# Optimization experiments

Measured on AMD Instinct MI355X. Metric: run time of the kernel, lower is better.

Reference implementation:

```python
import jax, jax.numpy as jnp
import numpy as np
from jax import lax

HIDDEN_DIM = 256


def _conv(x, w, b, stride):
    # x: [B,T,H,W,Cin], w: [1,kh,kw,Cin,Cout]
    y = lax.conv_general_dilated(
        x, w, window_strides=(1, stride, stride), padding='SAME',
        dimension_numbers=('NDHWC', 'DHWIO', 'NDHWC'))
    return y + b


def _encode(video, w1, b1, w2, b2, w3, b3):
    x = video / 255.0
    x = jax.nn.relu(_conv(x, w1, b1, 2))
    x = jax.nn.relu(_conv(x, w2, b2, 2))
    x = jax.nn.relu(_conv(x, w3, b3, 2))
    return x  # [B,T,H/8,W/8,HIDDEN_DIM]


def _sample_features(features, t_idx, y_idx, x_idx):
    # Bilinear sample features[b, t_idx, y_idx, x_idx] -> [B,N,C]
    B, T, H, W, C = features.shape
    t = jnp.clip(t_idx, 0, T - 1)
    y0 = jnp.clip(jnp.floor(y_idx).astype(jnp.int32), 0, H - 1)
    y1 = jnp.clip(y0 + 1, 0, H - 1)
    x0 = jnp.clip(jnp.floor(x_idx).astype(jnp.int32), 0, W - 1)
    x1 = jnp.clip(x0 + 1, 0, W - 1)
    wy1 = y_idx - y0.astype(features.dtype)
    wy0 = 1.0 - wy1
    wx1 = x_idx - x0.astype(features.dtype)
    wx0 = 1.0 - wx1
    bi = jnp.arange(B)[:, None]
    f00 = features[bi, t, y0, x0]
    f01 = features[bi, t, y0, x1]
    f10 = features[bi, t, y1, x0]
    f11 = features[bi, t, y1, x1]
    f0 = f00 * wx0[..., None] + f01 * wx1[..., None]
    f1 = f10 * wx0[..., None] + f11 * wx1[..., None]
    return f0 * wy0[..., None] + f1 * wy1[..., None]


def _forward(video, query_points, w1, b1, w2, b2, w3, b3):
    B, T, H, W, _ = video.shape
    N = query_points.shape[1]
    x = _encode(video, w1, b1, w2, b2, w3, b3)
    feat_H, feat_W = x.shape[2], x.shape[3]
    query_t = (query_points[:, :, 0] * (T - 1)).astype(jnp.int32)
    query_y = query_points[:, :, 1] * (feat_H - 1)
    query_x = query_points[:, :, 2] * (feat_W - 1)
    q = _sample_features(x, query_t, query_y, query_x)  # [B,N,C]
    # dense correlation volume [B,N,T,fH,fW]
    corr = jnp.einsum('bnc,bthwc->bnthw', q, x) / jnp.sqrt(jnp.float32(HIDDEN_DIM))
    probs = jax.nn.softmax(corr.reshape(B, N, T, feat_H * feat_W) * 10.0, axis=-1)
    yy, xx = jnp.meshgrid(jnp.arange(feat_H, dtype=x.dtype),
                          jnp.arange(feat_W, dtype=x.dtype), indexing='ij')
    coords_flat = jnp.stack([xx.flatten(), yy.flatten()], axis=-1)  # [fH*fW, 2]
    pred = jnp.einsum('bntk,kc->bntc', probs, coords_flat)
    pred = pred.at[..., 0].set(pred[..., 0] * (W / feat_W))
    pred = pred.at[..., 1].set(pred[..., 1] * (H / feat_H))
    occlusion = jax.nn.sigmoid(-jnp.max(corr, axis=(-2, -1)))  # [B,N,T]
    return pred, occlusion


def setup_inputs() -> dict:
    key = jax.random.key(0)
    ks = jax.random.split(key, 10)
    B, T, H, W, N = 2, 24, 256, 256, 512
    video = jax.random.uniform(ks[0], (B, T, H, W, 3), jnp.float32) * 255.0
    query_points = jax.random.uniform(ks[1], (B, N, 3), jnp.float32)
    s = 0.05
    w1 = jax.random.normal(ks[2], (1, 7, 7, 3, 64), jnp.float32) * s
    b1 = jnp.zeros((64,), jnp.float32)
    w2 = jax.random.normal(ks[3], (1, 3, 3, 64, 128), jnp.float32) * s
    b2 = jnp.zeros((128,), jnp.float32)
    w3 = jax.random.normal(ks[4], (1, 3, 3, 128, HIDDEN_DIM), jnp.float32) * s
    b3 = jnp.zeros((HIDDEN_DIM,), jnp.float32)
    return {'video': video, 'query_points': query_points,
            'w1': w1, 'b1': b1, 'w2': w2, 'b2': b2, 'w3': w3, 'b3': b3}


def reference(video, query_points, w1, b1, w2, b2, w3, b3):
    return _forward(video, query_points, w1, b1, w2, b2, w3, b3)
```

## Files before the change

### kernel.cpp

```cpp
#include <hip/hip_runtime.h>
#include <hip/hip_bf16.h>
#include <cstdint>
#include <cstddef>


typedef __attribute__((ext_vector_type(8))) short bf16x8;
typedef __attribute__((ext_vector_type(4))) float f32x4;

typedef const __attribute__((address_space(1))) void gv_t;
typedef __attribute__((address_space(3))) void sv_t;

__device__ __forceinline__ unsigned short bfr(float f) {
    return (unsigned short)(__bfloat16_as_ushort(__float2bfloat16(f)));
}

__global__ __launch_bounds__(256) void k_prep(const float* __restrict__ video,
                                              const float* __restrict__ w1,
                                              const float* __restrict__ w2,
                                              const float* __restrict__ w3,
                                              __hip_bfloat16* __restrict__ pv,
                                              unsigned short* __restrict__ c1p,
                                              unsigned short* __restrict__ c2p,
                                              __hip_bfloat16* __restrict__ wp1,
                                              __hip_bfloat16* __restrict__ wp2,
                                              __hip_bfloat16* __restrict__ wp3)
{
    const int bid = blockIdx.x;
    if (bid < 12288) {
        const int iy = bid & 255;
        const int bt = bid >> 8;
        const int ix = threadIdx.x;
        const float* src = video + ((size_t)(bt * 256 + iy) * 256 + ix) * 3;
        unsigned* dst = (unsigned*)(pv + ((size_t)(bt * 261) + iy + 2) * 1056);
        const float v0 = src[0], v1 = src[1], v2 = src[2];
        const unsigned lo = (unsigned)bfr(v0) | ((unsigned)bfr(v1) << 16);
        const unsigned hi = (unsigned)bfr(v2);
        dst[(2 + ix) * 2 + 0] = lo;
        dst[(2 + ix) * 2 + 1] = hi;
        if (ix < 2)   { dst[ix * 2] = 0u; dst[ix * 2 + 1] = 0u; }
        if (ix >= 250){ dst[(ix + 8) * 2] = 0u; dst[(ix + 8) * 2 + 1] = 0u; }
    } else if (bid < 12288 + 7170) {
        const int i = (bid - 12288) * 256 + threadIdx.x;
        unsigned short* pvs = (unsigned short*)pv;
        if (i < 253440) {
            const int bt = i / 5280, rr = (i % 5280) / 1056, col = i % 1056;
            const int row = (rr < 2) ? rr : rr + 256;
            pvs[(size_t)(bt * 261 + row) * 1056 + col] = 0;
        } else if (i < 1042944) {
            const int j = i - 253440, bt = j / 16448, k = j % 16448;
            size_t addr;
            if (k < 8256) { const int px = k >> 6, c = k & 63;
                addr = ((size_t)(bt * 129 + 128) * 129 + px) * 64 + c; }
            else { const int k2 = k - 8256, row = k2 >> 6, c = k2 & 63;
                addr = ((size_t)(bt * 129 + row) * 129 + 128) * 64 + c; }
            c1p[addr] = 0;
        } else if (i < 1835520) {
            const int j = i - 1042944, bt = j / 16512, k = j % 16512;
            size_t addr;
            if (k < 8320) { const int px = k >> 7, c = k & 127;
                addr = ((size_t)(bt * 65 + 64) * 65 + px) * 128 + c; }
            else { const int k2 = k - 8320, row = k2 >> 7, c = k2 & 127;
                addr = ((size_t)(bt * 65 + row) * 65 + 64) * 128 + c; }
            c2p[addr] = 0;
        }
    } else {
        const int e = (bid - 12288 - 7170) * 256 + threadIdx.x;
        if (e < 14336) {
            const int j = e & 7, lane = (e >> 3) & 63, nt = (e >> 9) & 3, kh = e >> 11;
            const int k = ((lane >> 4) << 3) + j;
            const int kw = k >> 2, ci = k & 3;
            const int n = nt * 16 + (lane & 15);
            float v = (ci < 3 && kw < 7) ? w1[(size_t)((kh * 7 + kw) * 3 + ci) * 64 + n] : 0.f;
            wp1[e] = __float2bfloat16(v);
        } else if (e < 88064) {
            const int e2 = e - 14336;
            const int j = e2 & 7, lane = (e2 >> 3) & 63, nt = (e2 >> 9) & 7, ks = (e2 >> 12) & 1, tap = e2 >> 13;
            const int ci = ks * 32 + ((lane >> 4) << 3) + j;
            const int n  = nt * 16 + (lane & 15);
            wp2[e2] = __float2bfloat16(w2[(size_t)(tap * 64 + ci) * 128 + n]);
        } else {
            const int e3 = e - 88064;
            const int j = e3 & 7, lane = (e3 >> 3) & 63, nt = (e3 >> 9) & 15, ks = (e3 >> 13) & 3, tap = e3 >> 15;
            const int ci = ks * 32 + ((lane >> 4) << 3) + j;
            const int n  = nt * 16 + (lane & 15);
            wp3[e3] = __float2bfloat16(w3[(size_t)(tap * 128 + ci) * 256 + n]);
        }
    }
}

__global__ __launch_bounds__(256) void k_conv1m(const __hip_bfloat16* __restrict__ pv,
                                                const __hip_bfloat16* __restrict__ wp,
                                                const float* __restrict__ b1,
                                                __hip_bfloat16* __restrict__ out)
{
    const int xcd = blockIdx.x & 7;
    const int sub = blockIdx.x >> 3;
    const int bt  = xcd * 6 + (sub >> 7);
    const int oy  = sub & 127;
    const int w  = threadIdx.x >> 6;
    const int l  = threadIdx.x & 63;
    const int li = l & 15, lh = l >> 4;

    f32x4 acc[2][4];
#pragma unroll
    for (int m = 0; m < 2; ++m)
#pragma unroll
        for (int n = 0; n < 4; ++n) acc[m][n] = (f32x4){0.f, 0.f, 0.f, 0.f};

    const short* pvS = (const short*)pv;
    const short* wS  = (const short*)wp;

#pragma unroll
    for (int kh = 0; kh < 7; ++kh) {
        const short* row = pvS + (size_t)(bt * 261 + oy * 2 + kh) * 1056;
        bf16x8 bw[4];
#pragma unroll
        for (int nt = 0; nt < 4; ++nt)
            bw[nt] = *reinterpret_cast<const bf16x8*>(wS + ((size_t)(kh * 4 + nt) * 64 + l) * 8);
#pragma unroll
        for (int mt = 0; mt < 2; ++mt) {
            const int ox = w * 32 + mt * 16 + li;
            bf16x8 a = *reinterpret_cast<const bf16x8*>(row + 8 * (ox + lh));
#pragma unroll
            for (int nt = 0; nt < 4; ++nt)
                acc[mt][nt] = __builtin_amdgcn_mfma_f32_16x16x32_bf16(a, bw[nt], acc[mt][nt], 0, 0, 0);
        }
    }

    __hip_bfloat16* op = out + ((size_t)(bt * 129 + oy) * 129) * 64;
#pragma unroll
    for (int mt = 0; mt < 2; ++mt) {
        const int px0 = w * 32 + mt * 16 + lh * 4;
#pragma unroll
        for (int nt = 0; nt < 4; ++nt) {
            const int n = nt * 16 + li;
            const float bias = b1[n];
#pragma unroll
            for (int r = 0; r < 4; ++r) {
                const float v = fmaxf(acc[mt][nt][r] * (1.f / 255.f) + bias, 0.f);
                op[(size_t)(px0 + r) * 64 + n] = __float2bfloat16(v);
            }
        }
    }
}

template<int CIN, int COUT, int OW, int IW, int ORS, int NTHR, int WMT, int WNT, int MINW>
__global__ __launch_bounds__(NTHR, MINW) void k_convr(const __hip_bfloat16* __restrict__ in,
                                                      const __hip_bfloat16* __restrict__ wp,
                                                      const float* __restrict__ bias,
                                                      __hip_bfloat16* __restrict__ out)
{
    constexpr int KSN  = CIN / 32;
    constexpr int NSL  = 9 * KSN;
    constexpr int NTT  = COUT / 16;
    constexpr int GPX  = CIN / 8;
    constexpr int ROWG = IW * GPX;
    constexpr int RST  = ROWG * 16;
    constexpr int TOT  = 3 * ROWG;
    constexpr int SIT  = (TOT + NTHR - 1) / NTHR;

    __shared__ char lbuf[3 * RST];

    const int bid = blockIdx.x;
    const int xcd = bid & 7;
    const int sub = bid >> 3;
    const int bt  = xcd * 6 + sub / OW;
    const int oy  = sub % OW;

    const int tid = threadIdx.x;
    const int w   = tid >> 6;
    const int l   = tid & 63;
    const int li  = l & 15, lh = l >> 4;
    const int ntb = w * WNT;

    const short* inS = (const short*)in;
    const size_t rb = (size_t)(bt * IW + oy * 2) * IW * CIN;
#pragma unroll
    for (int it = 0; it < SIT; ++it) {
        const int g = it * NTHR + tid;
        if (g < TOT) {
            const int r  = g / ROWG;
            const int rm = g - r * ROWG;
            const int px = rm / GPX;
            const int j  = rm - px * GPX;
            const int q  = j ^ ((px >> 1) & 7);
            __builtin_amdgcn_global_load_lds(
                (gv_t*)(inS + rb + (size_t)r * IW * CIN + px * CIN + q * 8),
                (sv_t*)(lbuf + (size_t)g * 16), 16, 0, 0);
        }
    }
    __syncthreads();

    f32x4 acc[WMT][WNT];
#pragma unroll
    for (int i = 0; i < WMT; ++i)
#pragma unroll
        for (int j = 0; j < WNT; ++j) acc[i][j] = (f32x4){0.f, 0.f, 0.f, 0.f};

    const char* wB = (const char*)wp;

#pragma unroll
    for (int s = 0; s < NSL; ++s) {
        const int tap = s / KSN, ks = s % KSN;
        const int kh = tap / 3, kw = tap % 3;

        bf16x8 bf[WNT];
#pragma unroll
        for (int j = 0; j < WNT; ++j)
            bf[j] = *reinterpret_cast<const bf16x8*>(wB + ((size_t)s * NTT + ntb + j) * 1024 + l * 16);

        const char* Ar = lbuf + kh * RST;
        bf16x8 af[WMT];
#pragma unroll
        for (int i = 0; i < WMT; ++i) {
            const int ix  = (i * 16 + li) * 2 + kw;
            const int off = ((ks * 4 + lh) ^ ((ix >> 1) & 7)) * 16;
            af[i] = *reinterpret_cast<const bf16x8*>(Ar + (size_t)ix * (CIN * 2) + off);
        }

#pragma unroll
        for (int i = 0; i < WMT; ++i)
#pragma unroll
            for (int j = 0; j < WNT; ++j)
                acc[i][j] = __builtin_amdgcn_mfma_f32_16x16x32_bf16(af[i], bf[j], acc[i][j], 0, 0, 0);
    }

    __hip_bfloat16* ob = out + (size_t)(bt * ORS + oy) * ORS * COUT;
#pragma unroll
    for (int i = 0; i < WMT; ++i) {
        const int ox = i * 16 + lh * 4;
#pragma unroll
        for (int j = 0; j < WNT; ++j) {
            const int n = (ntb + j) * 16 + li;
            const float bv = bias[n];
#pragma unroll
            for (int r = 0; r < 4; ++r) {
                const float v = fmaxf(acc[i][j][r] + bv, 0.f);
                ob[(size_t)(ox + r) * COUT + n] = __float2bfloat16(v);
            }
        }
    }
}

__global__ __launch_bounds__(256) void k_sample(const float* __restrict__ qp,
                                                const __hip_bfloat16* __restrict__ feat,
                                                __hip_bfloat16* __restrict__ q)
{
    const int bn = blockIdx.x;
    const int b  = bn >> 9;
    const float t3 = qp[bn * 3 + 0];
    const float yv = qp[bn * 3 + 1] * 31.f;
    const float xv = qp[bn * 3 + 2] * 31.f;
    int t = (int)(t3 * 23.f);
    t = min(max(t, 0), 23);
    int y0 = (int)floorf(yv); y0 = min(max(y0, 0), 31);
    const int y1 = min(y0 + 1, 31);
    int x0 = (int)floorf(xv); x0 = min(max(x0, 0), 31);
    const int x1 = min(x0 + 1, 31);
    const float wy1 = yv - (float)y0, wy0 = 1.f - wy1;
    const float wx1 = xv - (float)x0, wx0 = 1.f - wx1;

    const int c = threadIdx.x;
    const __hip_bfloat16* fb = feat + ((size_t)(b * 24 + t) * 1024) * 256;
    const float f00 = __bfloat162float(fb[(size_t)(y0 * 32 + x0) * 256 + c]);
    const float f01 = __bfloat162float(fb[(size_t)(y0 * 32 + x1) * 256 + c]);
    const float f10 = __bfloat162float(fb[(size_t)(y1 * 32 + x0) * 256 + c]);
    const float f11 = __bfloat162float(fb[(size_t)(y1 * 32 + x1) * 256 + c]);
    const float v = (f00 * wx0 + f01 * wx1) * wy0 + (f10 * wx0 + f11 * wx1) * wy1;
    q[(size_t)bn * 256 + c] = __float2bfloat16(v);
}

__global__ __launch_bounds__(256, 2) void k_corrm(const __hip_bfloat16* __restrict__ qb,
                                                  const __hip_bfloat16* __restrict__ featb,
                                                  float* __restrict__ pbuf)
{
    __shared__ short lbuf[2][8192];

    const int bid = blockIdx.x;
    const int xcd = bid & 7;
    const int sub = bid >> 3;
    const int grp = sub >> 5;
    const int prt = sub & 31;
    const int img = xcd * 6 + grp;
    const int bq  = img / 24, t = img % 24;
    const int nc  = prt & 3, ps = prt >> 2;

    const int tid = threadIdx.x;
    const int w   = tid >> 6;
    const int l   = tid & 63;
    const int li  = l & 15, lh = l >> 4;

    const short* qS = (const short*)qb;
    const short* fS = (const short*)featb + (size_t)img * 1024 * 256;
    const char*  tile0 = (const char*)(fS + (size_t)(ps * 128) * 256);

    const int q0 = nc * 128 + w * 32;
    bf16x8 aq[2][8];
#pragma unroll
    for (int mt = 0; mt < 2; ++mt)
#pragma unroll
        for (int ks = 0; ks < 8; ++ks)
            aq[mt][ks] = *reinterpret_cast<const bf16x8*>(
                qS + ((size_t)(bq * 512 + q0 + mt * 16 + li)) * 256 + ks * 32 + lh * 8);

    float m[2][4], s[2][4], sx[2][4], sy[2][4], dmx[2][4];
#pragma unroll
    for (int mt = 0; mt < 2; ++mt)
#pragma unroll
        for (int r = 0; r < 4; ++r) {
            m[mt][r] = -1e30f; s[mt][r] = 0.f; sx[mt][r] = 0.f; sy[mt][r] = 0.f; dmx[mt][r] = -1e30f;
        }

    bf16x8 stg[4];
#pragma unroll
    for (int i = 0; i < 4; ++i) {
        const int g = i * 256 + tid;
        const int pos = g >> 5, kb = (g & 31) * 16;
        stg[i] = *reinterpret_cast<const bf16x8*>(tile0 + (size_t)pos * 512 + kb);
    }
#pragma unroll
    for (int i = 0; i < 4; ++i) {
        const int g = i * 256 + tid;
        const int pos = g >> 5, kb = (g & 31) * 16;
        *reinterpret_cast<bf16x8*>((char*)&lbuf[0][0] + pos * 512 + (kb ^ ((pos & 7) << 4))) = stg[i];
    }
    __syncthreads();

#pragma unroll
    for (int st = 0; st < 4; ++st) {
        const int cur = st & 1;

        if (st < 3) {
            const char* tn = tile0 + (size_t)((st + 1) * 32) * 512;
#pragma unroll
            for (int i = 0; i < 4; ++i) {
                const int g = i * 256 + tid;
                const int pos = g >> 5, kb = (g & 31) * 16;
                stg[i] = *reinterpret_cast<const bf16x8*>(tn + (size_t)pos * 512 + kb);
            }
        }

        f32x4 acc[2][2];
#pragma unroll
        for (int mt = 0; mt < 2; ++mt)
#pragma unroll
            for (int pt = 0; pt < 2; ++pt) acc[mt][pt] = (f32x4){0.f, 0.f, 0.f, 0.f};

#pragma unroll
        for (int pt = 0; pt < 2; ++pt) {
            const int p = pt * 16 + li;
#pragma unroll
            for (int ks = 0; ks < 8; ++ks) {
                const int k = ks * 32 + lh * 8;
                bf16x8 bv = *reinterpret_cast<const bf16x8*>(&lbuf[cur][p * 256 + (k ^ ((p & 7) << 3))]);
                acc[0][pt] = __builtin_amdgcn_mfma_f32_16x16x32_bf16(aq[0][ks], bv, acc[0][pt], 0, 0, 0);
                acc[1][pt] = __builtin_amdgcn_mfma_f32_16x16x32_bf16(aq[1][ks], bv, acc[1][pt], 0, 0, 0);
            }
        }

        const float py = (float)(ps * 4 + st);
#pragma unroll
        for (int mt = 0; mt < 2; ++mt)
#pragma unroll
            for (int r = 0; r < 4; ++r) {
                const float v0 = acc[mt][0][r], v1 = acc[mt][1][r];
                float mx = fmaxf(v0, v1);
                mx = fmaxf(mx, __shfl_xor(mx, 1));
                mx = fmaxf(mx, __shfl_xor(mx, 2));
                mx = fmaxf(mx, __shfl_xor(mx, 4));
                mx = fmaxf(mx, __shfl_xor(mx, 8));
                dmx[mt][r] = fmaxf(dmx[mt][r], mx);
                const float mn = fmaxf(m[mt][r], mx * 0.625f);
                const float sc = __expf(m[mt][r] - mn);
                const float e0 = __expf(v0 * 0.625f - mn);
                const float e1 = __expf(v1 * 0.625f - mn);
                const float es = e0 + e1;
                s[mt][r]  = s[mt][r]  * sc + es;
                sx[mt][r] = sx[mt][r] * sc + es * (float)li + 16.f * e1;
                sy[mt][r] = sy[mt][r] * sc + es * py;
                m[mt][r] = mn;
            }

        if (st < 3) {
#pragma unroll
            for (int i = 0; i < 4; ++i) {
                const int g = i * 256 + tid;
                const int pos = g >> 5, kb = (g & 31) * 16;
                *reinterpret_cast<bf16x8*>((char*)&lbuf[cur ^ 1][0] + pos * 512 + (kb ^ ((pos & 7) << 4))) = stg[i];
            }
            __syncthreads();
        }
    }

#pragma unroll
    for (int mt = 0; mt < 2; ++mt)
#pragma unroll
        for (int r = 0; r < 4; ++r) {
#pragma unroll
            for (int off = 1; off < 16; off <<= 1) {
                s[mt][r]  += __shfl_xor(s[mt][r],  off);
                sx[mt][r] += __shfl_xor(sx[mt][r], off);
                sy[mt][r] += __shfl_xor(sy[mt][r], off);
            }
        }

    if (li == 0) {
#pragma unroll
        for (int mt = 0; mt < 2; ++mt)
#pragma unroll
            for (int r = 0; r < 4; ++r) {
                const int n = q0 + mt * 16 + lh * 4 + r;
                const int bnt = (bq * 512 + n) * 24 + t;
                const int pi = ps * 24576 + bnt;
                pbuf[pi]                = m[mt][r];
                pbuf[196608 + pi]       = s[mt][r];
                pbuf[393216 + pi]       = sx[mt][r];
                pbuf[589824 + pi]       = sy[mt][r];
                pbuf[786432 + pi]       = dmx[mt][r];
            }
    }
}

__global__ __launch_bounds__(256) void k_merge(const float* __restrict__ pbuf,
                                               float* __restrict__ outp)
{
    const int i = blockIdx.x * 256 + threadIdx.x;
    float M = -1e30f, D = -1e30f;
#pragma unroll
    for (int ps = 0; ps < 8; ++ps) {
        M = fmaxf(M, pbuf[ps * 24576 + i]);
        D = fmaxf(D, pbuf[786432 + ps * 24576 + i]);
    }
    float s = 0.f, sx = 0.f, sy = 0.f;
#pragma unroll
    for (int ps = 0; ps < 8; ++ps) {
        const int pi = ps * 24576 + i;
        const float wgt = __expf(pbuf[pi] - M);
        s  += pbuf[196608 + pi] * wgt;
        sx += pbuf[393216 + pi] * wgt;
        sy += pbuf[589824 + pi] * wgt;
    }
    const float inv = 8.f / s;
    outp[i * 2 + 0] = sx * inv;
    outp[i * 2 + 1] = sy * inv;
    outp[49152 + i] = 1.f / (1.f + __expf(D * 0.0625f));
}

extern "C" void kernel_launch(void* const* d_in, const int* in_sizes, int n_in,
                              void* d_out, int out_size, void* d_ws, size_t ws_size,
                              hipStream_t stream)
{
    const float* video = (const float*)d_in[0];
    const float* qp    = (const float*)d_in[1];
    const float* w1    = (const float*)d_in[2];
    const float* b1    = (const float*)d_in[3];
    const float* w2    = (const float*)d_in[4];
    const float* b2    = (const float*)d_in[5];
    const float* w3    = (const float*)d_in[6];
    const float* b3    = (const float*)d_in[7];
    float* out = (float*)d_out;

    char* wsb = (char*)d_ws;
    __hip_bfloat16* c1p   = (__hip_bfloat16*)(wsb);
    __hip_bfloat16* c2p   = (__hip_bfloat16*)(wsb + 102242304ull);
    __hip_bfloat16* pv    = (__hip_bfloat16*)(wsb + 154159104ull);
    __hip_bfloat16* featb = (__hip_bfloat16*)(wsb + 154159104ull);
    __hip_bfloat16* qbuf  = (__hip_bfloat16*)(wsb + 180618240ull);
    __hip_bfloat16* w1p   = (__hip_bfloat16*)(wsb + 181142528ull);
    __hip_bfloat16* w2p   = (__hip_bfloat16*)(wsb + 181171200ull);
    __hip_bfloat16* w3p   = (__hip_bfloat16*)(wsb + 181318656ull);
    float*          pbuf  = (float*)(wsb + 181908480ull);

    k_prep      <<<dim3(20954),    dim3(256), 0, stream>>>(
                       video, w1, w2, w3, pv,
                       (unsigned short*)c1p, (unsigned short*)c2p, w1p, w2p, w3p);
    k_conv1m    <<<dim3(48 * 128), dim3(256), 0, stream>>>(pv, w1p, b1, c1p);
    k_convr<64, 128, 64, 129, 65, 256, 4, 2, 3><<<dim3(3072), dim3(256), 0, stream>>>(c1p, w2p, b2, c2p);
    k_convr<128, 256, 32, 65, 32, 512, 2, 2, 6><<<dim3(1536), dim3(512), 0, stream>>>(c2p, w3p, b3, featb);
    k_sample    <<<dim3(1024),     dim3(256), 0, stream>>>(qp, featb, qbuf);
    k_corrm     <<<dim3(1536),     dim3(256), 0, stream>>>(qbuf, featb, pbuf);
    k_merge     <<<dim3(96),       dim3(256), 0, stream>>>(pbuf, out);
}
```

Before: 189.7 us.

## Fuse conv1 and conv2 into one kernel staging conv1 rows in LDS

Conv1 and conv2 now run in one kernel. Each block computes the three conv1 output rows one conv2 output row needs and keeps them in swizzled shared memory, then runs the conv2 MFMA loop from LDS. This drops the round trip of the roughly 100 MB conv1 intermediate through global memory, plus its padding init and one launch. In exchange, conv1 rows that neighbouring output rows share (stride 2 with a 3-row window) are recomputed, roughly 1.5x the conv1 work, and about 48 KB of LDS per block limits occupancy.

```diff
diff --git a/kernel.cpp b/kernel.cpp
--- a/kernel.cpp
+++ b/kernel.cpp
@@ -19,7 +19,6 @@
                                               const float* __restrict__ w2,
                                               const float* __restrict__ w3,
                                               __hip_bfloat16* __restrict__ pv,
-                                              unsigned short* __restrict__ c1p,
                                               unsigned short* __restrict__ c2p,
                                               __hip_bfloat16* __restrict__ wp1,
                                               __hip_bfloat16* __restrict__ wp2,
@@ -39,23 +38,15 @@
         dst[(2 + ix) * 2 + 1] = hi;
         if (ix < 2)   { dst[ix * 2] = 0u; dst[ix * 2 + 1] = 0u; }
         if (ix >= 250){ dst[(ix + 8) * 2] = 0u; dst[(ix + 8) * 2 + 1] = 0u; }
-    } else if (bid < 12288 + 7170) {
+    } else if (bid < 12288 + 4086) {
         const int i = (bid - 12288) * 256 + threadIdx.x;
         unsigned short* pvs = (unsigned short*)pv;
         if (i < 253440) {
             const int bt = i / 5280, rr = (i % 5280) / 1056, col = i % 1056;
             const int row = (rr < 2) ? rr : rr + 256;
             pvs[(size_t)(bt * 261 + row) * 1056 + col] = 0;
-        } else if (i < 1042944) {
-            const int j = i - 253440, bt = j / 16448, k = j % 16448;
-            size_t addr;
-            if (k < 8256) { const int px = k >> 6, c = k & 63;
-                addr = ((size_t)(bt * 129 + 128) * 129 + px) * 64 + c; }
-            else { const int k2 = k - 8256, row = k2 >> 6, c = k2 & 63;
-                addr = ((size_t)(bt * 129 + row) * 129 + 128) * 64 + c; }
-            c1p[addr] = 0;
-        } else if (i < 1835520) {
-            const int j = i - 1042944, bt = j / 16512, k = j % 16512;
+        } else {
+            const int j = i - 253440, bt = j / 16512, k = j % 16512;
             size_t addr;
             if (k < 8320) { const int px = k >> 7, c = k & 127;
                 addr = ((size_t)(bt * 65 + 64) * 65 + px) * 128 + c; }
@@ -64,7 +55,7 @@
             c2p[addr] = 0;
         }
     } else {
-        const int e = (bid - 12288 - 7170) * 256 + threadIdx.x;
+        const int e = (bid - 12288 - 4086) * 256 + threadIdx.x;
         if (e < 14336) {
             const int j = e & 7, lane = (e >> 3) & 63, nt = (e >> 9) & 3, kh = e >> 11;
             const int k = ((lane >> 4) << 3) + j;
@@ -88,57 +79,130 @@
     }
 }
 
-__global__ __launch_bounds__(256) void k_conv1m(const __hip_bfloat16* __restrict__ pv,
-                                                const __hip_bfloat16* __restrict__ wp,
-                                                const float* __restrict__ b1,
-                                                __hip_bfloat16* __restrict__ out)
-{
+__global__ __launch_bounds__(256, 3) void k_conv12(const __hip_bfloat16* __restrict__ pv,
+                                                   const __hip_bfloat16* __restrict__ w1p,
+                                                   const float* __restrict__ b1,
+                                                   const __hip_bfloat16* __restrict__ w2p,
+                                                   const float* __restrict__ b2,
+                                                   __hip_bfloat16* __restrict__ c2p)
+{
+    __shared__ __align__(16) char lc1[3 * 16512];
+
     const int xcd = blockIdx.x & 7;
     const int sub = blockIdx.x >> 3;
-    const int bt  = xcd * 6 + (sub >> 7);
-    const int oy  = sub & 127;
-    const int w  = threadIdx.x >> 6;
-    const int l  = threadIdx.x & 63;
-    const int li = l & 15, lh = l >> 4;
-
-    f32x4 acc[2][4];
-#pragma unroll
-    for (int m = 0; m < 2; ++m)
-#pragma unroll
-        for (int n = 0; n < 4; ++n) acc[m][n] = (f32x4){0.f, 0.f, 0.f, 0.f};
+    const int bt  = xcd * 6 + sub / 64;
+    const int oy2 = sub % 64;
+    const int tid = threadIdx.x;
+    const int w   = tid >> 6;
+    const int l   = tid & 63;
+    const int li  = l & 15, lh = l >> 4;
 
     const short* pvS = (const short*)pv;
-    const short* wS  = (const short*)wp;
-
-#pragma unroll
-    for (int kh = 0; kh < 7; ++kh) {
-        const short* row = pvS + (size_t)(bt * 261 + oy * 2 + kh) * 1056;
-        bf16x8 bw[4];
-#pragma unroll
-        for (int nt = 0; nt < 4; ++nt)
-            bw[nt] = *reinterpret_cast<const bf16x8*>(wS + ((size_t)(kh * 4 + nt) * 64 + l) * 8);
-#pragma unroll
-        for (int mt = 0; mt < 2; ++mt) {
-            const int ox = w * 32 + mt * 16 + li;
-            bf16x8 a = *reinterpret_cast<const bf16x8*>(row + 8 * (ox + lh));
-#pragma unroll
-            for (int nt = 0; nt < 4; ++nt)
-                acc[mt][nt] = __builtin_amdgcn_mfma_f32_16x16x32_bf16(a, bw[nt], acc[mt][nt], 0, 0, 0);
-        }
-    }
-
-    __hip_bfloat16* op = out + ((size_t)(bt * 129 + oy) * 129) * 64;
-#pragma unroll
-    for (int mt = 0; mt < 2; ++mt) {
-        const int px0 = w * 32 + mt * 16 + lh * 4;
-#pragma unroll
-        for (int nt = 0; nt < 4; ++nt) {
-            const int n = nt * 16 + li;
-            const float bias = b1[n];
-#pragma unroll
-            for (int r = 0; r < 4; ++r) {
-                const float v = fmaxf(acc[mt][nt][r] * (1.f / 255.f) + bias, 0.f);
-                op[(size_t)(px0 + r) * 64 + n] = __float2bfloat16(v);
+    const short* w1S = (const short*)w1p;
+
+#pragma unroll
+    for (int kh2 = 0; kh2 < 3; ++kh2) {
+        const int r = oy2 * 2 + kh2;
+        char* rowbuf = lc1 + kh2 * 16512;
+        if (r < 128) {
+            f32x4 acc[2][4];
+#pragma unroll
+            for (int m = 0; m < 2; ++m)
+#pragma unroll
+                for (int n = 0; n < 4; ++n) acc[m][n] = (f32x4){0.f, 0.f, 0.f, 0.f};
+
+            const short* rbase = pvS + (size_t)(bt * 261 + r * 2) * 1056;
+#pragma unroll
+            for (int kh = 0; kh < 7; ++kh) {
+                bf16x8 bw[4];
+#pragma unroll
+                for (int nt = 0; nt < 4; ++nt)
+                    bw[nt] = *reinterpret_cast<const bf16x8*>(w1S + ((size_t)(kh * 4 + nt) * 64 + l) * 8);
+#pragma unroll
+                for (int mt = 0; mt < 2; ++mt) {
+                    bf16x8 a = *reinterpret_cast<const bf16x8*>(
+                        rbase + (size_t)kh * 1056 + 8 * (w * 32 + mt * 16 + li + lh));
+#pragma unroll
+                    for (int nt = 0; nt < 4; ++nt)
+                        acc[mt][nt] = __builtin_amdgcn_mfma_f32_16x16x32_bf16(a, bw[nt], acc[mt][nt], 0, 0, 0);
+                }
+            }
+#pragma unroll
+            for (int mt = 0; mt < 2; ++mt) {
+#pragma unroll
+                for (int nt = 0; nt < 4; ++nt) {
+                    const int n = nt * 16 + li;
+                    const float bias = b1[n];
+                    const int jg = nt * 2 + (li >> 3);
+#pragma unroll
+                    for (int r4 = 0; r4 < 4; ++r4) {
+                        const int px = w * 32 + mt * 16 + lh * 4 + r4;
+                        const float v = fmaxf(acc[mt][nt][r4] * (1.f / 255.f) + bias, 0.f);
+                        *reinterpret_cast<unsigned short*>(
+                            rowbuf + px * 128 + ((jg ^ ((px >> 1) & 7)) * 16 + (li & 7) * 2)) = bfr(v);
+                    }
+                }
+            }
+            if (tid < 8)
+                *reinterpret_cast<uint4*>(rowbuf + 128 * 128 + tid * 16) = (uint4){0u, 0u, 0u, 0u};
+        } else {
+#pragma unroll
+            for (int it = 0; it < 5; ++it) {
+                const int g = it * 256 + tid;
+                if (g < 1032)
+                    *reinterpret_cast<uint4*>(rowbuf + (size_t)g * 16) = (uint4){0u, 0u, 0u, 0u};
+            }
+        }
+    }
+    __syncthreads();
+
+    const int ntb = w * 2;
+    f32x4 acc[4][2];
+#pragma unroll
+    for (int i = 0; i < 4; ++i) {
+        acc[i][0] = (f32x4){0.f, 0.f, 0.f, 0.f};
+        acc[i][1] = (f32x4){0.f, 0.f, 0.f, 0.f};
+    }
+
+    const char* wB = (const char*)w2p;
+#pragma unroll
+    for (int s = 0; s < 18; ++s) {
+        const int tap = s >> 1, ks = s & 1;
+        const int kh = tap / 3, kw = tap % 3;
+
+        bf16x8 bf[2];
+#pragma unroll
+        for (int j = 0; j < 2; ++j)
+            bf[j] = *reinterpret_cast<const bf16x8*>(wB + ((size_t)s * 8 + ntb + j) * 1024 + l * 16);
+
+        const char* Ar = lc1 + kh * 16512;
+        bf16x8 af[4];
+#pragma unroll
+        for (int i = 0; i < 4; ++i) {
+            const int ix  = (i * 16 + li) * 2 + kw;
+            const int off = ((ks * 4 + lh) ^ ((ix >> 1) & 7)) * 16;
+            af[i] = *reinterpret_cast<const bf16x8*>(Ar + (size_t)ix * 128 + off);
+        }
+
+#pragma unroll
+        for (int i = 0; i < 4; ++i)
+#pragma unroll
+            for (int j = 0; j < 2; ++j)
+                acc[i][j] = __builtin_amdgcn_mfma_f32_16x16x32_bf16(af[i], bf[j], acc[i][j], 0, 0, 0);
+    }
+
+    __hip_bfloat16* ob = c2p + (size_t)(bt * 65 + oy2) * 65 * 128;
+#pragma unroll
+    for (int i = 0; i < 4; ++i) {
+        const int ox = i * 16 + lh * 4;
+#pragma unroll
+        for (int j = 0; j < 2; ++j) {
+            const int n = (ntb + j) * 16 + li;
+            const float bv = b2[n];
+#pragma unroll
+            for (int r4 = 0; r4 < 4; ++r4) {
+                const float v = fmaxf(acc[i][j][r4] + bv, 0.f);
+                ob[(size_t)(ox + r4) * 128 + n] = __float2bfloat16(v);
             }
         }
     }
@@ -461,23 +525,20 @@
     float* out = (float*)d_out;
 
     char* wsb = (char*)d_ws;
-    __hip_bfloat16* c1p   = (__hip_bfloat16*)(wsb);
-    __hip_bfloat16* c2p   = (__hip_bfloat16*)(wsb + 102242304ull);
-    __hip_bfloat16* pv    = (__hip_bfloat16*)(wsb + 154159104ull);
-    __hip_bfloat16* featb = (__hip_bfloat16*)(wsb + 154159104ull);
-    __hip_bfloat16* qbuf  = (__hip_bfloat16*)(wsb + 180618240ull);
-    __hip_bfloat16* w1p   = (__hip_bfloat16*)(wsb + 181142528ull);
-    __hip_bfloat16* w2p   = (__hip_bfloat16*)(wsb + 181171200ull);
-    __hip_bfloat16* w3p   = (__hip_bfloat16*)(wsb + 181318656ull);
-    float*          pbuf  = (float*)(wsb + 181908480ull);
-
-    k_prep      <<<dim3(20954),    dim3(256), 0, stream>>>(
-                       video, w1, w2, w3, pv,
-                       (unsigned short*)c1p, (unsigned short*)c2p, w1p, w2p, w3p);
-    k_conv1m    <<<dim3(48 * 128), dim3(256), 0, stream>>>(pv, w1p, b1, c1p);
-    k_convr<64, 128, 64, 129, 65, 256, 4, 2, 3><<<dim3(3072), dim3(256), 0, stream>>>(c1p, w2p, b2, c2p);
+    __hip_bfloat16* c2p   = (__hip_bfloat16*)(wsb);
+    __hip_bfloat16* pv    = (__hip_bfloat16*)(wsb + 51916800ull);
+    __hip_bfloat16* featb = (__hip_bfloat16*)(wsb + 51916800ull);
+    __hip_bfloat16* qbuf  = (__hip_bfloat16*)(wsb + 78375936ull);
+    __hip_bfloat16* w1p   = (__hip_bfloat16*)(wsb + 78900224ull);
+    __hip_bfloat16* w2p   = (__hip_bfloat16*)(wsb + 78928896ull);
+    __hip_bfloat16* w3p   = (__hip_bfloat16*)(wsb + 79076352ull);
+    float*          pbuf  = (float*)(wsb + 79666176ull);
+
+    k_prep   <<<dim3(17870), dim3(256), 0, stream>>>(
+                  video, w1, w2, w3, pv, (unsigned short*)c2p, w1p, w2p, w3p);
+    k_conv12 <<<dim3(3072),  dim3(256), 0, stream>>>(pv, w1p, b1, w2p, b2, c2p);
     k_convr<128, 256, 32, 65, 32, 512, 2, 2, 6><<<dim3(1536), dim3(512), 0, stream>>>(c2p, w3p, b3, featb);
-    k_sample    <<<dim3(1024),     dim3(256), 0, stream>>>(qp, featb, qbuf);
-    k_corrm     <<<dim3(1536),     dim3(256), 0, stream>>>(qbuf, featb, pbuf);
-    k_merge     <<<dim3(96),       dim3(256), 0, stream>>>(pbuf, out);
-}
+    k_sample <<<dim3(1024),  dim3(256), 0, stream>>>(qp, featb, qbuf);
+    k_corrm  <<<dim3(1536),  dim3(256), 0, stream>>>(qbuf, featb, pbuf);
+    k_merge  <<<dim3(96),    dim3(256), 0, stream>>>(pbuf, out);
+}
```

Result: faster. 180.5 us (-4.9%).
